# Optimization experiments

Measured on AMD Instinct MI355X. Metric: run time of the kernel, lower is better.

## Reference

```python
import jax, jax.numpy as jnp
import numpy as np
import math

D_MODEL = 1024
N_HEADS = 16
B, L, K = 2, 512, 4


def sinusoidal_pe(n, dim):
    # matches SinusoidalEmbedding buffer pe[:n]
    position = jnp.arange(n, dtype=jnp.float32)[:, None]
    div_term = jnp.exp(jnp.arange(0, dim, 2, dtype=jnp.float32) * (-math.log(10000.0) / dim))
    ang = position * div_term  # [n, dim//2]
    pe = jnp.zeros((n, dim), dtype=jnp.float32)
    pe = pe.at[:, 0::2].set(jnp.sin(ang))
    pe = pe.at[:, 1::2].set(jnp.cos(ang))
    return pe


def setup_inputs() -> dict:
    key = jax.random.key(0)
    ks = jax.random.split(key, 8)
    s = 1.0 / math.sqrt(D_MODEL)
    return {
        "h": jax.random.normal(ks[0], (B, L, K, D_MODEL), dtype=jnp.float32),
        "probs": jax.random.uniform(ks[1], (B, L, K), dtype=jnp.float32),
        "Wq": jax.random.normal(ks[2], (D_MODEL, D_MODEL), dtype=jnp.float32) * s,
        "bq": jnp.zeros((D_MODEL,), dtype=jnp.float32),
        "Wk": jax.random.normal(ks[3], (D_MODEL, D_MODEL), dtype=jnp.float32) * s,
        "bk": jnp.zeros((D_MODEL,), dtype=jnp.float32),
        "Wv": jax.random.normal(ks[4], (D_MODEL, D_MODEL), dtype=jnp.float32) * s,
        "bv": jnp.zeros((D_MODEL,), dtype=jnp.float32),
        "Wo": jax.random.normal(ks[5], (D_MODEL, D_MODEL), dtype=jnp.float32) * s,
        "bo": jnp.zeros((D_MODEL,), dtype=jnp.float32),
        "prob_bias_scale": jnp.float32(1.0),
        "n_heads": N_HEADS,
    }


def reference(h, probs, Wq, bq, Wk, bk, Wv, bv, Wo, bo, prob_bias_scale, n_heads):
    Bh, Lh, kh, D = h.shape
    N = Lh * kh
    hd = D // n_heads
    scale = hd ** (-0.5)

    h_flat = h.reshape(Bh, N, D) + sinusoidal_pe(N, D)[None]  # [B, N, D]
    probs_flat = probs.reshape(Bh, N)

    # torch Linear: x @ W.T + b
    q = (h_flat @ Wq.T + bq).reshape(Bh, N, n_heads, hd).transpose(0, 2, 1, 3)
    key = (h_flat @ Wk.T + bk).reshape(Bh, N, n_heads, hd).transpose(0, 2, 1, 3)
    v = (h_flat @ Wv.T + bv).reshape(Bh, N, n_heads, hd).transpose(0, 2, 1, 3)

    scores = jnp.einsum("bhnd,bhmd->bhnm", q, key) * scale  # [B,H,N,N]
    prob_bias = jnp.log(probs_flat + 1e-8)[:, None, None, :]  # bias on key axis
    scores = scores + prob_bias_scale * prob_bias
    attn = jax.nn.softmax(scores, axis=-1)  # dropout is identity in eval
    out = jnp.einsum("bhnm,bhmd->bhnd", attn, v)
    out = out.transpose(0, 2, 1, 3).reshape(Bh, N, D)
    out = out @ Wo.T + bo
    return out.reshape(Bh, Lh, kh, D)
```

## Files before the change

### kernel.cpp

```cpp
#include <hip/hip_runtime.h>

typedef _Float16 h8 __attribute__((ext_vector_type(8)));
typedef float f32x4 __attribute__((ext_vector_type(4)));

#define NSEQ 2048
#define DMODEL 1024
#define HD 64
#define C2 0.1803368801111244f

#define OFF_HPE  (size_t)0
#define OFF_WQ   (size_t)8388608
#define OFF_WK   (size_t)10485760
#define OFF_WV   (size_t)12582912
#define OFF_WO   (size_t)14680064
#define OFF_Q    (size_t)16777216
#define OFF_K    (size_t)25165824
#define OFF_VT   (size_t)33554432
#define OFF_AO   (size_t)41943040
#define OFF_PB   (size_t)50331648

#define GLL(g, l) __builtin_amdgcn_global_load_lds( \
    (const __attribute__((address_space(1))) unsigned int*)(const void*)(g), \
    (__attribute__((address_space(3))) unsigned int*)(l), 16, 0, 0)

__global__ void hpe_kernel(const float* __restrict__ h, _Float16* __restrict__ hpe) {
    int idx = blockIdx.x * blockDim.x + threadIdx.x;
    int row = idx >> 9;
    int i2  = idx & 511;
    int n = row & (NSEQ - 1);
    const float kTerm = -9.210340371976184f / 1024.0f;
    float div = expf((float)(2 * i2) * kTerm);
    float ang = (float)n * div;
    float s = sinf(ang), c = cosf(ang);
    int base = row * DMODEL + 2 * i2;
    hpe[base]     = (_Float16)(h[base] + s);
    hpe[base + 1] = (_Float16)(h[base + 1] + c);
}

__global__ void cast_kernel(const float* __restrict__ src, _Float16* __restrict__ dst) {
    int i = blockIdx.x * blockDim.x + threadIdx.x;
    float4 v = ((const float4*)src)[i];
    union { _Float16 hh[4]; uint2 u; } o;
    o.hh[0] = (_Float16)v.x; o.hh[1] = (_Float16)v.y;
    o.hh[2] = (_Float16)v.z; o.hh[3] = (_Float16)v.w;
    ((uint2*)dst)[i] = o.u;
}

__global__ void pb_kernel(const float* __restrict__ probs, const float* __restrict__ pbs,
                          float* __restrict__ pb) {
    int i = blockIdx.x * blockDim.x + threadIdx.x;
    pb[i] = pbs[0] * log2f(probs[i] + 1e-8f);
}

#define GBM 128
#define GBN 64

template<int MODE>
__global__ __launch_bounds__(256) void gemm_nt(
    const _Float16* __restrict__ A, const _Float16* __restrict__ W,
    const float* __restrict__ bias, void* __restrict__ Cout)
{
    __shared__ __align__(16) _Float16 As[GBM][64];
    __shared__ __align__(16) _Float16 Bs[GBN][64];
    int tm = blockIdx.x * GBM;
    int tn = blockIdx.y * GBN;
    int t = threadIdx.x;
    int wave = t >> 6, lane = t & 63;
    int wr = (wave >> 1) * 64, wc = (wave & 1) * 32;
    int lr = lane & 15, lg = lane >> 4;

    f32x4 acc[4][2] = {};

    int grow = lane >> 3;
    int gcol = (lane & 7) * 8;
    const _Float16* Aptr = A + (size_t)(tm + wave * 8 + grow) * DMODEL + gcol;
    const _Float16* Wptr = W + (size_t)(tn + wave * 8 + grow) * DMODEL + gcol;

    for (int k0 = 0; k0 < DMODEL; k0 += 64) {
        __syncthreads();
        #pragma unroll
        for (int i = 0; i < 4; ++i)
            GLL(Aptr + (size_t)i * 32 * DMODEL + k0, &As[i * 32 + wave * 8][0]);
        #pragma unroll
        for (int i = 0; i < 2; ++i)
            GLL(Wptr + (size_t)i * 32 * DMODEL + k0, &Bs[i * 32 + wave * 8][0]);
        __syncthreads();
        #pragma unroll
        for (int kk = 0; kk < 2; ++kk) {
            h8 af[4], bf[2];
            #pragma unroll
            for (int mi = 0; mi < 4; ++mi) af[mi] = *(const h8*)&As[wr + mi * 16 + lr][kk * 32 + lg * 8];
            #pragma unroll
            for (int ni = 0; ni < 2; ++ni) bf[ni] = *(const h8*)&Bs[wc + ni * 16 + lr][kk * 32 + lg * 8];
            #pragma unroll
            for (int mi = 0; mi < 4; ++mi)
                #pragma unroll
                for (int ni = 0; ni < 2; ++ni)
                    acc[mi][ni] = __builtin_amdgcn_mfma_f32_16x16x32_f16(af[mi], bf[ni], acc[mi][ni], 0, 0, 0);
        }
    }

    #pragma unroll
    for (int mi = 0; mi < 4; ++mi)
        #pragma unroll
        for (int ni = 0; ni < 2; ++ni)
            #pragma unroll
            for (int j = 0; j < 4; ++j) {
                int row = tm + wr + mi * 16 + lg * 4 + j;
                int col = tn + wc + ni * 16 + lr;
                float v = acc[mi][ni][j] + bias[col];
                if (MODE == 0) {
                    ((_Float16*)Cout)[(size_t)row * DMODEL + col] = (_Float16)v;
                } else if (MODE == 1) {
                    int b = row >> 11, nn = row & 2047;
                    ((_Float16*)Cout)[((size_t)b * 1024 + col) * 2048 + nn] = (_Float16)v;
                } else {
                    ((float*)Cout)[(size_t)row * DMODEL + col] = v;
                }
            }
}

#define QT 64
#define KT 64

__global__ __launch_bounds__(256, 4) void flash_kernel(
    const _Float16* __restrict__ Qb,
    const _Float16* __restrict__ Kb,
    const _Float16* __restrict__ Vt,
    const float* __restrict__ pb,
    _Float16* __restrict__ AO)
{
    __shared__ __align__(16) _Float16 Ks[KT][72];
    __shared__ __align__(16) _Float16 Vs[HD][72];
    __shared__ __align__(16) _Float16 Ps[4][16][72];
    int bh = blockIdx.y;
    int b = bh >> 4, h = bh & 15;
    int q0 = blockIdx.x * QT;
    int t = threadIdx.x, wave = t >> 6, lane = t & 63;
    int lr = lane & 15, lg = lane >> 4;

    const _Float16* Khead  = Kb + (size_t)b * NSEQ * DMODEL + h * HD;
    const _Float16* Vthead = Vt + ((size_t)b * 1024 + h * HD) * NSEQ;
    const float* pbb = pb + b * NSEQ;

    const _Float16* Qrow = Qb + ((size_t)b * NSEQ + q0 + wave * 16 + lr) * DMODEL + h * HD;
    h8 qf0 = *(const h8*)&Qrow[lg * 8];
    h8 qf1 = *(const h8*)&Qrow[32 + lg * 8];

    float mrun = -INFINITY, lrun = 0.f;
    f32x4 oacc[4] = {};

    int srow = t >> 2, sc = (t & 3) * 16;

    for (int k0 = 0; k0 < NSEQ; k0 += KT) {
        f32x4 pbv[4];
        #pragma unroll
        for (int ci = 0; ci < 4; ++ci)
            pbv[ci] = *(const f32x4*)&pbb[k0 + ci * 16 + lg * 4];

        __syncthreads();
        *(h8*)&Ks[srow][sc]     = *(const h8*)&Khead[(size_t)(k0 + srow) * DMODEL + sc];
        *(h8*)&Ks[srow][sc + 8] = *(const h8*)&Khead[(size_t)(k0 + srow) * DMODEL + sc + 8];
        *(h8*)&Vs[srow][sc]     = *(const h8*)&Vthead[(size_t)srow * NSEQ + k0 + sc];
        *(h8*)&Vs[srow][sc + 8] = *(const h8*)&Vthead[(size_t)srow * NSEQ + k0 + sc + 8];
        __syncthreads();

        f32x4 s[4] = {};
        #pragma unroll
        for (int ci = 0; ci < 4; ++ci) {
            h8 kf = *(const h8*)&Ks[ci * 16 + lr][lg * 8];
            s[ci] = __builtin_amdgcn_mfma_f32_16x16x32_f16(kf, qf0, s[ci], 0, 0, 0);
        }
        #pragma unroll
        for (int ci = 0; ci < 4; ++ci) {
            h8 kf = *(const h8*)&Ks[ci * 16 + lr][32 + lg * 8];
            s[ci] = __builtin_amdgcn_mfma_f32_16x16x32_f16(kf, qf1, s[ci], 0, 0, 0);
        }

        float p[4][4];
        float sm = -INFINITY;
        #pragma unroll
        for (int ci = 0; ci < 4; ++ci)
            #pragma unroll
            for (int j = 0; j < 4; ++j) {
                float vv = fmaf(s[ci][j], C2, pbv[ci][j]);
                p[ci][j] = vv;
                sm = fmaxf(sm, vv);
            }
        sm = fmaxf(sm, __shfl_xor(sm, 16));
        sm = fmaxf(sm, __shfl_xor(sm, 32));
        float newm = fmaxf(mrun, sm);
        float fs = __builtin_amdgcn_exp2f(mrun - newm);
        float rs = 0.f;
        #pragma unroll
        for (int ci = 0; ci < 4; ++ci)
            #pragma unroll
            for (int j = 0; j < 4; ++j) {
                float e = __builtin_amdgcn_exp2f(p[ci][j] - newm);
                p[ci][j] = e;
                rs += e;
            }
        rs += __shfl_xor(rs, 16);
        rs += __shfl_xor(rs, 32);
        lrun = lrun * fs + rs;
        mrun = newm;

        #pragma unroll
        for (int ci = 0; ci < 4; ++ci) {
            union { _Float16 hh[4]; uint2 u; } pk;
            #pragma unroll
            for (int j = 0; j < 4; ++j) pk.hh[j] = (_Float16)p[ci][j];
            *(uint2*)&Ps[wave][lr][ci * 16 + lg * 4] = pk.u;
        }
        asm volatile("s_waitcnt lgkmcnt(0)" ::: "memory");
        __builtin_amdgcn_sched_barrier(0);

        #pragma unroll
        for (int j = 0; j < 4; ++j) {
            float fsj = __shfl(fs, (lane & 48) | (lg * 4 + j), 64);
            #pragma unroll
            for (int ni = 0; ni < 4; ++ni) oacc[ni][j] *= fsj;
        }

        #pragma unroll
        for (int kb = 0; kb < 2; ++kb) {
            h8 pa = *(const h8*)&Ps[wave][lr][kb * 32 + lg * 8];
            #pragma unroll
            for (int ni = 0; ni < 4; ++ni) {
                h8 vf = *(const h8*)&Vs[ni * 16 + lr][kb * 32 + lg * 8];
                oacc[ni] = __builtin_amdgcn_mfma_f32_16x16x32_f16(pa, vf, oacc[ni], 0, 0, 0);
            }
        }
    }

    #pragma unroll
    for (int j = 0; j < 4; ++j) {
        float lj = __shfl(lrun, (lane & 48) | (lg * 4 + j), 64);
        float inv = 1.0f / lj;
        int row = q0 + wave * 16 + lg * 4 + j;
        #pragma unroll
        for (int ni = 0; ni < 4; ++ni)
            AO[((size_t)b * NSEQ + row) * DMODEL + h * HD + ni * 16 + lr] = (_Float16)(oacc[ni][j] * inv);
    }
}

extern "C" void kernel_launch(void* const* d_in, const int* in_sizes, int n_in,
                              void* d_out, int out_size, void* d_ws, size_t ws_size,
                              hipStream_t stream) {
    const float* h    = (const float*)d_in[0];
    const float* prob = (const float*)d_in[1];
    const float* Wq   = (const float*)d_in[2];
    const float* bq   = (const float*)d_in[3];
    const float* Wk   = (const float*)d_in[4];
    const float* bk   = (const float*)d_in[5];
    const float* Wv   = (const float*)d_in[6];
    const float* bv   = (const float*)d_in[7];
    const float* Wo   = (const float*)d_in[8];
    const float* bo   = (const float*)d_in[9];
    const float* pbs  = (const float*)d_in[10];

    char* ws = (char*)d_ws;
    _Float16* hpe  = (_Float16*)(ws + OFF_HPE);
    _Float16* wq16 = (_Float16*)(ws + OFF_WQ);
    _Float16* wk16 = (_Float16*)(ws + OFF_WK);
    _Float16* wv16 = (_Float16*)(ws + OFF_WV);
    _Float16* wo16 = (_Float16*)(ws + OFF_WO);
    _Float16* qb   = (_Float16*)(ws + OFF_Q);
    _Float16* kb16 = (_Float16*)(ws + OFF_K);
    _Float16* vt   = (_Float16*)(ws + OFF_VT);
    _Float16* ao   = (_Float16*)(ws + OFF_AO);
    float*    pbuf = (float*)(ws + OFF_PB);

    hpe_kernel<<<dim3(8192), dim3(256), 0, stream>>>(h, hpe);
    cast_kernel<<<dim3(1024), dim3(256), 0, stream>>>(Wq, wq16);
    cast_kernel<<<dim3(1024), dim3(256), 0, stream>>>(Wk, wk16);
    cast_kernel<<<dim3(1024), dim3(256), 0, stream>>>(Wv, wv16);
    cast_kernel<<<dim3(1024), dim3(256), 0, stream>>>(Wo, wo16);
    pb_kernel<<<dim3(16), dim3(256), 0, stream>>>(prob, pbs, pbuf);

    gemm_nt<0><<<dim3(32, 16), dim3(256), 0, stream>>>(hpe, wq16, bq, qb);
    gemm_nt<0><<<dim3(32, 16), dim3(256), 0, stream>>>(hpe, wk16, bk, kb16);
    gemm_nt<1><<<dim3(32, 16), dim3(256), 0, stream>>>(hpe, wv16, bv, vt);

    flash_kernel<<<dim3(32, 32), dim3(256), 0, stream>>>(qb, kb16, vt, pbuf, ao);

    gemm_nt<2><<<dim3(32, 16), dim3(256), 0, stream>>>(ao, wo16, bo, d_out);
}
```

Before: 264.9 us.

## Fuse QKV GEMMs and weight casts, swizzle flash LDS, keep P in registers

Merges the four weight-cast launches into one kernel and the three QKV projections into a single launch with 128x128 tiles, writing the transposed V with packed 4-wide stores. The output projection gets its own 64x128-tiled kernel. In the flash kernel, K and V tiles move to an XOR-swizzled unpadded LDS layout to avoid bank conflicts. When the 16x16x16 MFMA builtin exists, the P tile feeds the PV MFMA straight from registers, which removes the per-wave LDS round trip for P. The costs are more MFMA instructions of the smaller shape and higher register pressure in the larger GEMM tiles.

```diff
diff --git a/kernel.cpp b/kernel.cpp
--- a/kernel.cpp
+++ b/kernel.cpp
@@ -1,6 +1,7 @@
 #include <hip/hip_runtime.h>
 
 typedef _Float16 h8 __attribute__((ext_vector_type(8)));
+typedef _Float16 h4 __attribute__((ext_vector_type(4)));
 typedef float f32x4 __attribute__((ext_vector_type(4)));
 
 #define NSEQ 2048
@@ -22,6 +23,12 @@
 #define GLL(g, l) __builtin_amdgcn_global_load_lds( \
     (const __attribute__((address_space(1))) unsigned int*)(const void*)(g), \
     (__attribute__((address_space(3))) unsigned int*)(l), 16, 0, 0)
+
+#if __has_builtin(__builtin_amdgcn_mfma_f32_16x16x16f16)
+#define HAVE_MFMA16 1
+#else
+#define HAVE_MFMA16 0
+#endif
 
 __global__ void hpe_kernel(const float* __restrict__ h, _Float16* __restrict__ hpe) {
     int idx = blockIdx.x * blockDim.x + threadIdx.x;
@@ -37,13 +44,19 @@
     hpe[base + 1] = (_Float16)(h[base + 1] + c);
 }
 
-__global__ void cast_kernel(const float* __restrict__ src, _Float16* __restrict__ dst) {
+__global__ void cast4_kernel(const float* __restrict__ w0, const float* __restrict__ w1,
+                             const float* __restrict__ w2, const float* __restrict__ w3,
+                             _Float16* __restrict__ d0, _Float16* __restrict__ d1,
+                             _Float16* __restrict__ d2, _Float16* __restrict__ d3) {
     int i = blockIdx.x * blockDim.x + threadIdx.x;
-    float4 v = ((const float4*)src)[i];
+    int which = i >> 18, idx = i & 262143;
+    const float* s = which == 0 ? w0 : which == 1 ? w1 : which == 2 ? w2 : w3;
+    _Float16* d    = which == 0 ? d0 : which == 1 ? d1 : which == 2 ? d2 : d3;
+    float4 v = ((const float4*)s)[idx];
     union { _Float16 hh[4]; uint2 u; } o;
     o.hh[0] = (_Float16)v.x; o.hh[1] = (_Float16)v.y;
     o.hh[2] = (_Float16)v.z; o.hh[3] = (_Float16)v.w;
-    ((uint2*)dst)[i] = o.u;
+    ((uint2*)d)[idx] = o.u;
 }
 
 __global__ void pb_kernel(const float* __restrict__ probs, const float* __restrict__ pbs,
@@ -52,24 +65,25 @@
     pb[i] = pbs[0] * log2f(probs[i] + 1e-8f);
 }
 
-#define GBM 128
-#define GBN 64
-
-template<int MODE>
-__global__ __launch_bounds__(256) void gemm_nt(
-    const _Float16* __restrict__ A, const _Float16* __restrict__ W,
-    const float* __restrict__ bias, void* __restrict__ Cout)
+__global__ __launch_bounds__(256) void gemm_qkv(
+    const _Float16* __restrict__ A,
+    const _Float16* __restrict__ Wqp, const _Float16* __restrict__ Wkp, const _Float16* __restrict__ Wvp,
+    const float* __restrict__ bqp, const float* __restrict__ bkp, const float* __restrict__ bvp,
+    _Float16* __restrict__ qb, _Float16* __restrict__ kb, _Float16* __restrict__ vt)
 {
-    __shared__ __align__(16) _Float16 As[GBM][64];
-    __shared__ __align__(16) _Float16 Bs[GBN][64];
-    int tm = blockIdx.x * GBM;
-    int tn = blockIdx.y * GBN;
+    __shared__ __align__(16) _Float16 As[128][64];
+    __shared__ __align__(16) _Float16 Bs[128][64];
+    int widx = blockIdx.y >> 3;
+    const _Float16* W = widx == 0 ? Wqp : widx == 1 ? Wkp : Wvp;
+    const float* bias = widx == 0 ? bqp : widx == 1 ? bkp : bvp;
+    int tm = blockIdx.x * 128;
+    int tn = (blockIdx.y & 7) * 128;
     int t = threadIdx.x;
     int wave = t >> 6, lane = t & 63;
-    int wr = (wave >> 1) * 64, wc = (wave & 1) * 32;
+    int wr = (wave >> 1) * 64, wc = (wave & 1) * 64;
     int lr = lane & 15, lg = lane >> 4;
 
-    f32x4 acc[4][2] = {};
+    f32x4 acc[4][4] = {};
 
     int grow = lane >> 3;
     int gcol = (lane & 7) * 8;
@@ -82,20 +96,20 @@
         for (int i = 0; i < 4; ++i)
             GLL(Aptr + (size_t)i * 32 * DMODEL + k0, &As[i * 32 + wave * 8][0]);
         #pragma unroll
-        for (int i = 0; i < 2; ++i)
+        for (int i = 0; i < 4; ++i)
             GLL(Wptr + (size_t)i * 32 * DMODEL + k0, &Bs[i * 32 + wave * 8][0]);
         __syncthreads();
         #pragma unroll
         for (int kk = 0; kk < 2; ++kk) {
-            h8 af[4], bf[2];
+            h8 af[4], bf[4];
             #pragma unroll
             for (int mi = 0; mi < 4; ++mi) af[mi] = *(const h8*)&As[wr + mi * 16 + lr][kk * 32 + lg * 8];
             #pragma unroll
-            for (int ni = 0; ni < 2; ++ni) bf[ni] = *(const h8*)&Bs[wc + ni * 16 + lr][kk * 32 + lg * 8];
+            for (int ni = 0; ni < 4; ++ni) bf[ni] = *(const h8*)&Bs[wc + ni * 16 + lr][kk * 32 + lg * 8];
             #pragma unroll
             for (int mi = 0; mi < 4; ++mi)
                 #pragma unroll
-                for (int ni = 0; ni < 2; ++ni)
+                for (int ni = 0; ni < 4; ++ni)
                     acc[mi][ni] = __builtin_amdgcn_mfma_f32_16x16x32_f16(af[mi], bf[ni], acc[mi][ni], 0, 0, 0);
         }
     }
@@ -103,25 +117,87 @@
     #pragma unroll
     for (int mi = 0; mi < 4; ++mi)
         #pragma unroll
-        for (int ni = 0; ni < 2; ++ni)
+        for (int ni = 0; ni < 4; ++ni) {
+            int col = tn + wc + ni * 16 + lr;
+            float bv = bias[col];
+            if (widx < 2) {
+                _Float16* dst = widx == 0 ? qb : kb;
+                #pragma unroll
+                for (int j = 0; j < 4; ++j) {
+                    int row = tm + wr + mi * 16 + lg * 4 + j;
+                    dst[(size_t)row * DMODEL + col] = (_Float16)(acc[mi][ni][j] + bv);
+                }
+            } else {
+                int row0 = tm + wr + mi * 16 + lg * 4;
+                int b = row0 >> 11, n0 = row0 & 2047;
+                h4 pk;
+                #pragma unroll
+                for (int j = 0; j < 4; ++j) pk[j] = (_Float16)(acc[mi][ni][j] + bv);
+                *(h4*)&vt[((size_t)b * 1024 + col) * 2048 + n0] = pk;
+            }
+        }
+}
+
+__global__ __launch_bounds__(256) void gemm_ao(
+    const _Float16* __restrict__ A, const _Float16* __restrict__ W,
+    const float* __restrict__ bias, float* __restrict__ C)
+{
+    __shared__ __align__(16) _Float16 As[64][64];
+    __shared__ __align__(16) _Float16 Bs[128][64];
+    int tm = blockIdx.x * 64;
+    int tn = blockIdx.y * 128;
+    int t = threadIdx.x;
+    int wave = t >> 6, lane = t & 63;
+    int wr = (wave >> 1) * 32, wc = (wave & 1) * 64;
+    int lr = lane & 15, lg = lane >> 4;
+
+    f32x4 acc[2][4] = {};
+
+    int grow = lane >> 3;
+    int gcol = (lane & 7) * 8;
+    const _Float16* Aptr = A + (size_t)(tm + wave * 8 + grow) * DMODEL + gcol;
+    const _Float16* Wptr = W + (size_t)(tn + wave * 8 + grow) * DMODEL + gcol;
+
+    for (int k0 = 0; k0 < DMODEL; k0 += 64) {
+        __syncthreads();
+        #pragma unroll
+        for (int i = 0; i < 2; ++i)
+            GLL(Aptr + (size_t)i * 32 * DMODEL + k0, &As[i * 32 + wave * 8][0]);
+        #pragma unroll
+        for (int i = 0; i < 4; ++i)
+            GLL(Wptr + (size_t)i * 32 * DMODEL + k0, &Bs[i * 32 + wave * 8][0]);
+        __syncthreads();
+        #pragma unroll
+        for (int kk = 0; kk < 2; ++kk) {
+            h8 af[2], bf[4];
+            #pragma unroll
+            for (int mi = 0; mi < 2; ++mi) af[mi] = *(const h8*)&As[wr + mi * 16 + lr][kk * 32 + lg * 8];
+            #pragma unroll
+            for (int ni = 0; ni < 4; ++ni) bf[ni] = *(const h8*)&Bs[wc + ni * 16 + lr][kk * 32 + lg * 8];
+            #pragma unroll
+            for (int mi = 0; mi < 2; ++mi)
+                #pragma unroll
+                for (int ni = 0; ni < 4; ++ni)
+                    acc[mi][ni] = __builtin_amdgcn_mfma_f32_16x16x32_f16(af[mi], bf[ni], acc[mi][ni], 0, 0, 0);
+        }
+    }
+
+    #pragma unroll
+    for (int mi = 0; mi < 2; ++mi)
+        #pragma unroll
+        for (int ni = 0; ni < 4; ++ni)
             #pragma unroll
             for (int j = 0; j < 4; ++j) {
                 int row = tm + wr + mi * 16 + lg * 4 + j;
                 int col = tn + wc + ni * 16 + lr;
-                float v = acc[mi][ni][j] + bias[col];
-                if (MODE == 0) {
-                    ((_Float16*)Cout)[(size_t)row * DMODEL + col] = (_Float16)v;
-                } else if (MODE == 1) {
-                    int b = row >> 11, nn = row & 2047;
-                    ((_Float16*)Cout)[((size_t)b * 1024 + col) * 2048 + nn] = (_Float16)v;
-                } else {
-                    ((float*)Cout)[(size_t)row * DMODEL + col] = v;
-                }
+                C[(size_t)row * DMODEL + col] = acc[mi][ni][j] + bias[col];
             }
 }
 
 #define QT 64
 #define KT 64
+
+#define SWZ(row, bytecol) ((row) * 128 + ((bytecol) ^ (((row) & 7) << 4)))
 
 __global__ __launch_bounds__(256, 4) void flash_kernel(
     const _Float16* __restrict__ Qb,
@@ -130,9 +206,11 @@
     const float* __restrict__ pb,
     _Float16* __restrict__ AO)
 {
-    __shared__ __align__(16) _Float16 Ks[KT][72];
-    __shared__ __align__(16) _Float16 Vs[HD][72];
+    __shared__ __align__(16) char KsB[64 * 128];
+    __shared__ __align__(16) char VsB[64 * 128];
+#if !HAVE_MFMA16
     __shared__ __align__(16) _Float16 Ps[4][16][72];
+#endif
     int bh = blockIdx.y;
     int b = bh >> 4, h = bh & 15;
     int q0 = blockIdx.x * QT;
@@ -150,7 +228,8 @@
     float mrun = -INFINITY, lrun = 0.f;
     f32x4 oacc[4] = {};
 
-    int srow = t >> 2, sc = (t & 3) * 16;
+    int srow = t >> 2;
+    int sc = (t & 3) * 32;
 
     for (int k0 = 0; k0 < NSEQ; k0 += KT) {
         f32x4 pbv[4];
@@ -159,21 +238,21 @@
             pbv[ci] = *(const f32x4*)&pbb[k0 + ci * 16 + lg * 4];
 
         __syncthreads();
-        *(h8*)&Ks[srow][sc]     = *(const h8*)&Khead[(size_t)(k0 + srow) * DMODEL + sc];
-        *(h8*)&Ks[srow][sc + 8] = *(const h8*)&Khead[(size_t)(k0 + srow) * DMODEL + sc + 8];
-        *(h8*)&Vs[srow][sc]     = *(const h8*)&Vthead[(size_t)srow * NSEQ + k0 + sc];
-        *(h8*)&Vs[srow][sc + 8] = *(const h8*)&Vthead[(size_t)srow * NSEQ + k0 + sc + 8];
+        *(h8*)(KsB + SWZ(srow, sc))      = *(const h8*)&Khead[(size_t)(k0 + srow) * DMODEL + (sc >> 1)];
+        *(h8*)(KsB + SWZ(srow, sc + 16)) = *(const h8*)&Khead[(size_t)(k0 + srow) * DMODEL + (sc >> 1) + 8];
+        *(h8*)(VsB + SWZ(srow, sc))      = *(const h8*)&Vthead[(size_t)srow * NSEQ + k0 + (sc >> 1)];
+        *(h8*)(VsB + SWZ(srow, sc + 16)) = *(const h8*)&Vthead[(size_t)srow * NSEQ + k0 + (sc >> 1) + 8];
         __syncthreads();
 
         f32x4 s[4] = {};
         #pragma unroll
         for (int ci = 0; ci < 4; ++ci) {
-            h8 kf = *(const h8*)&Ks[ci * 16 + lr][lg * 8];
+            h8 kf = *(const h8*)(KsB + SWZ(ci * 16 + lr, lg * 16));
             s[ci] = __builtin_amdgcn_mfma_f32_16x16x32_f16(kf, qf0, s[ci], 0, 0, 0);
         }
         #pragma unroll
         for (int ci = 0; ci < 4; ++ci) {
-            h8 kf = *(const h8*)&Ks[ci * 16 + lr][32 + lg * 8];
+            h8 kf = *(const h8*)(KsB + SWZ(ci * 16 + lr, 64 + lg * 16));
             s[ci] = __builtin_amdgcn_mfma_f32_16x16x32_f16(kf, qf1, s[ci], 0, 0, 0);
         }
 
@@ -206,6 +285,26 @@
         mrun = newm;
 
         #pragma unroll
+        for (int j = 0; j < 4; ++j) {
+            float fsj = __shfl(fs, (lane & 48) | (lg * 4 + j), 64);
+            #pragma unroll
+            for (int ni = 0; ni < 4; ++ni) oacc[ni][j] *= fsj;
+        }
+
+#if HAVE_MFMA16
+        #pragma unroll
+        for (int ci = 0; ci < 4; ++ci) {
+            h4 pa;
+            #pragma unroll
+            for (int j = 0; j < 4; ++j) pa[j] = (_Float16)p[ci][j];
+            #pragma unroll
+            for (int ni = 0; ni < 4; ++ni) {
+                h4 vf = *(const h4*)(VsB + SWZ(ni * 16 + lr, ci * 32 + lg * 8));
+                oacc[ni] = __builtin_amdgcn_mfma_f32_16x16x16f16(pa, vf, oacc[ni], 0, 0, 0);
+            }
+        }
+#else
+        #pragma unroll
         for (int ci = 0; ci < 4; ++ci) {
             union { _Float16 hh[4]; uint2 u; } pk;
             #pragma unroll
@@ -214,23 +313,16 @@
         }
         asm volatile("s_waitcnt lgkmcnt(0)" ::: "memory");
         __builtin_amdgcn_sched_barrier(0);
-
-        #pragma unroll
-        for (int j = 0; j < 4; ++j) {
-            float fsj = __shfl(fs, (lane & 48) | (lg * 4 + j), 64);
-            #pragma unroll
-            for (int ni = 0; ni < 4; ++ni) oacc[ni][j] *= fsj;
-        }
-
-        #pragma unroll
-        for (int kb = 0; kb < 2; ++kb) {
-            h8 pa = *(const h8*)&Ps[wave][lr][kb * 32 + lg * 8];
+        #pragma unroll
+        for (int kb2 = 0; kb2 < 2; ++kb2) {
+            h8 pa = *(const h8*)&Ps[wave][lr][kb2 * 32 + lg * 8];
             #pragma unroll
             for (int ni = 0; ni < 4; ++ni) {
-                h8 vf = *(const h8*)&Vs[ni * 16 + lr][kb * 32 + lg * 8];
+                h8 vf = *(const h8*)(VsB + SWZ(ni * 16 + lr, kb2 * 64 + lg * 16));
                 oacc[ni] = __builtin_amdgcn_mfma_f32_16x16x32_f16(pa, vf, oacc[ni], 0, 0, 0);
             }
         }
+#endif
     }
 
     #pragma unroll
@@ -272,17 +364,12 @@
     float*    pbuf = (float*)(ws + OFF_PB);
 
     hpe_kernel<<<dim3(8192), dim3(256), 0, stream>>>(h, hpe);
-    cast_kernel<<<dim3(1024), dim3(256), 0, stream>>>(Wq, wq16);
-    cast_kernel<<<dim3(1024), dim3(256), 0, stream>>>(Wk, wk16);
-    cast_kernel<<<dim3(1024), dim3(256), 0, stream>>>(Wv, wv16);
-    cast_kernel<<<dim3(1024), dim3(256), 0, stream>>>(Wo, wo16);
+    cast4_kernel<<<dim3(4096), dim3(256), 0, stream>>>(Wq, Wk, Wv, Wo, wq16, wk16, wv16, wo16);
     pb_kernel<<<dim3(16), dim3(256), 0, stream>>>(prob, pbs, pbuf);
 
-    gemm_nt<0><<<dim3(32, 16), dim3(256), 0, stream>>>(hpe, wq16, bq, qb);
-    gemm_nt<0><<<dim3(32, 16), dim3(256), 0, stream>>>(hpe, wk16, bk, kb16);
-    gemm_nt<1><<<dim3(32, 16), dim3(256), 0, stream>>>(hpe, wv16, bv, vt);
+    gemm_qkv<<<dim3(32, 24), dim3(256), 0, stream>>>(hpe, wq16, wk16, wv16, bq, bk, bv, qb, kb16, vt);
 
     flash_kernel<<<dim3(32, 32), dim3(256), 0, stream>>>(qb, kb16, vt, pbuf, ao);
 
-    gemm_nt<2><<<dim3(32, 16), dim3(256), 0, stream>>>(ao, wo16, bo, d_out);
-}
+    gemm_ao<<<dim3(64, 8), dim3(256), 0, stream>>>(ao, wo16, bo, (float*)d_out);
+}
```

Result: faster. 247.1 us (-6.7%).
